# Kernel optimization log

Hardware: AMD Instinct MI355X
Metric: run time of the kernel (lower is better)

The kernel has to match this reference:

```python
import jax, jax.numpy as jnp
import numpy as np

N_NODES = 50000
N_EDGES = 800000
N_GRAPHS = 128
D = 128
L = 4
C = 10
GN_EPS = 1e-5


def setup_inputs() -> dict:
    key = jax.random.key(0)
    ks = jax.random.split(key, 12)
    s = 0.05
    x = jax.random.normal(ks[0], (N_NODES, D), dtype=jnp.float32)
    gin_w1 = jax.random.normal(ks[1], (L, D, D), dtype=jnp.float32) * s
    gin_b1 = jax.random.normal(ks[2], (L, D), dtype=jnp.float32) * s
    gin_w2 = jax.random.normal(ks[3], (L, D, D), dtype=jnp.float32) * s
    gin_b2 = jax.random.normal(ks[4], (L, D), dtype=jnp.float32) * s
    gn_weight = jnp.ones((L, D), dtype=jnp.float32)
    gn_bias = jnp.zeros((L, D), dtype=jnp.float32)
    gn_scale = jnp.ones((L, D), dtype=jnp.float32)
    fw1 = jax.random.normal(ks[5], (D, D), dtype=jnp.float32) * s
    fb1 = jnp.zeros((D,), dtype=jnp.float32)
    fw2 = jax.random.normal(ks[6], (D, D), dtype=jnp.float32) * s
    fb2 = jnp.zeros((D,), dtype=jnp.float32)
    fw3 = jax.random.normal(ks[7], (D, C), dtype=jnp.float32) * s
    fb3 = jnp.zeros((C,), dtype=jnp.float32)
    edge_index = jax.random.randint(ks[8], (2, N_EDGES), 0, N_NODES, dtype=jnp.int64)
    batch = jnp.sort(jax.random.randint(ks[9], (N_NODES,), 0, N_GRAPHS, dtype=jnp.int64))
    return dict(x=x, gin_w1=gin_w1, gin_b1=gin_b1, gin_w2=gin_w2, gin_b2=gin_b2,
                gn_weight=gn_weight, gn_bias=gn_bias, gn_scale=gn_scale,
                fw1=fw1, fb1=fb1, fw2=fw2, fb2=fb2, fw3=fw3, fb3=fb3,
                edge_index=edge_index, batch=batch)


def _graph_norm(h, batch, weight, bias, mean_scale, counts):
    # PyG GraphNorm: per-graph mean/var with learnable mean_scale.
    mean = jax.ops.segment_sum(h, batch, num_segments=N_GRAPHS) / counts  # [G, D]
    out = h - mean[batch] * mean_scale
    var = jax.ops.segment_sum(out * out, batch, num_segments=N_GRAPHS) / counts
    return weight * out / jnp.sqrt(var[batch] + GN_EPS) + bias


def reference(x, gin_w1, gin_b1, gin_w2, gin_b2, gn_weight, gn_bias, gn_scale,
              fw1, fb1, fw2, fb2, fw3, fb3, edge_index, batch):
    src, dst = edge_index[0], edge_index[1]
    ones = jnp.ones((N_NODES, 1), dtype=x.dtype)
    counts = jnp.maximum(jax.ops.segment_sum(ones, batch, num_segments=N_GRAPHS), 1.0)  # [G,1]
    h = x
    for l in range(L):
        # GINConv, eps=0: (1+eps)*x + sum_{j->i} x_j, then MLP with act after each Linear
        agg = jax.ops.segment_sum(h[src], dst, num_segments=N_NODES)  # [N, D]
        h = h + agg
        h = jax.nn.relu(h @ gin_w1[l] + gin_b1[l])
        h = jax.nn.relu(h @ gin_w2[l] + gin_b2[l])
        h = _graph_norm(h, batch, gn_weight[l], gn_bias[l], gn_scale[l], counts)
        h = jax.nn.relu(h)
    # sum readout per graph
    g = jax.ops.segment_sum(h, batch, num_segments=N_GRAPHS)  # [G, D]
    # final MLP (dropout is identity in eval)
    g = jax.nn.relu(g @ fw1 + fb1)
    g = jax.nn.relu(g @ fw2 + fb2)
    out = g @ fw3 + fb3
    return jax.nn.log_softmax(out, axis=-1)
```

## Files before the change

kernel.cpp:

```cpp
#include <hip/hip_runtime.h>
#include <cstddef>

#define N_NODES 50000
#define N_EDGES 800000
#define N_GRAPHS 128
#define DIM 128
#define N_LAYERS 4
#define GN_EPS 1e-5f

#define B_CHUNK 256
#define EPB 3125
#define BUCKET_SHIFT 9
#define BUCKET_SIZE 512
#define NB 98

#define CX_BLKS 12500
#define CW_BLKS 512
#define GB_BLKS 196
#define SETUP_BLKS (CX_BLKS + CW_BLKS + GB_BLKS + B_CHUNK)

typedef unsigned short ushort_t;
typedef __attribute__((ext_vector_type(8))) short frag8;
typedef __attribute__((ext_vector_type(4))) float f32x4;

__device__ inline float bfbits2f(unsigned hi16) { return __uint_as_float(hi16 << 16); }
__device__ inline ushort_t bf16rne(float v) {
    unsigned u = __float_as_uint(v);
    unsigned r = u + 0x7fff + ((u >> 16) & 1);
    return (ushort_t)(r >> 16);
}
__device__ inline unsigned packbf2(float a, float b) {
    return (unsigned)bf16rne(a) | ((unsigned)bf16rne(b) << 16);
}
__device__ inline void bf16split(float v, ushort_t& h, ushort_t& l) {
    ushort_t hi = bf16rne(v);
    float fh = __uint_as_float(((unsigned)hi) << 16);
    l = bf16rne(v - fh);
    h = hi;
}

__global__ __launch_bounds__(256) void setup_misc(const float* __restrict__ x, unsigned* __restrict__ Hb,
                                                  const float* __restrict__ w1, const float* __restrict__ w2,
                                                  ushort_t* __restrict__ whi, ushort_t* __restrict__ wlo,
                                                  const int* __restrict__ batch, int* __restrict__ gstart,
                                                  const int* __restrict__ edst, int* __restrict__ cnts) {
    __shared__ int cnt[NB];
    int b = blockIdx.x, t = threadIdx.x;
    if (b < CX_BLKS) {
        int i = b * 256 + t;
        if (i < N_NODES * 64) {
            float a = x[2 * i], bb = x[2 * i + 1];
            Hb[i] = packbf2(a, bb);
        }
    } else if (b < CX_BLKS + CW_BLKS) {
        int idx = (b - CX_BLKS) * 256 + t;
        int mat = idx >> 14;
        int e = idx & 16383;
        int n = e >> 7, k = e & 127;
        int l = mat >> 1;
        const float* src = (mat & 1) ? (w2 + (size_t)l * DIM * DIM) : (w1 + (size_t)l * DIM * DIM);
        float v = src[k * DIM + n];
        ushort_t h, lw;
        bf16split(v, h, lw);
        whi[(size_t)mat * DIM * DIM + n * DIM + k] = h;
        wlo[(size_t)mat * DIM * DIM + n * DIM + k] = lw;
    } else if (b < CX_BLKS + CW_BLKS + GB_BLKS) {
        int i = (b - CX_BLKS - CW_BLKS) * 256 + t;
        if (i < N_NODES) {
            int bb = batch[i];
            if (i == 0) {
                for (int g = 0; g <= bb; ++g) gstart[g] = 0;
            } else {
                int pb = batch[i - 1];
                for (int g = pb + 1; g <= bb; ++g) gstart[g] = i;
            }
            if (i == N_NODES - 1) {
                for (int g = bb + 1; g <= N_GRAPHS; ++g) gstart[g] = N_NODES;
            }
        }
    } else {
        int blk = b - (CX_BLKS + CW_BLKS + GB_BLKS);
        for (int i = t; i < NB; i += 256) cnt[i] = 0;
        __syncthreads();
        int base = blk * EPB;
        for (int i = t; i < EPB; i += 256) atomicAdd(&cnt[edst[base + i] >> BUCKET_SHIFT], 1);
        __syncthreads();
        for (int i = t; i < NB; i += 256) cnts[i * B_CHUNK + blk] = cnt[i];
    }
}

__global__ __launch_bounds__(1024) void scan_local(const int* __restrict__ in, int* __restrict__ out,
                                                   int* __restrict__ bsum, int n) {
    __shared__ int wsum[16];
    int tid = threadIdx.x, lane = tid & 63, w = tid >> 6;
    int gi = blockIdx.x * 1024 + tid;
    int v = (gi < n) ? in[gi] : 0;
    int s = v;
    #pragma unroll
    for (int off = 1; off < 64; off <<= 1) {
        int t = __shfl_up(s, off, 64);
        if (lane >= off) s += t;
    }
    if (lane == 63) wsum[w] = s;
    __syncthreads();
    if (w == 0) {
        int ws = (lane < 16) ? wsum[lane] : 0;
        #pragma unroll
        for (int off = 1; off < 16; off <<= 1) {
            int t = __shfl_up(ws, off, 64);
            if (lane >= off) ws += t;
        }
        if (lane < 16) wsum[lane] = ws;
    }
    __syncthreads();
    int woff = (w > 0) ? wsum[w - 1] : 0;
    if (gi < n) out[gi] = woff + s - v;
    if (tid == 1023) bsum[blockIdx.x] = woff + s;
}

__global__ __launch_bounds__(1024) void scan_add(int* __restrict__ out, const int* __restrict__ bsum,
                                                 int n, int total) {
    int lane = threadIdx.x & 63;
    int v = (lane < (int)blockIdx.x) ? bsum[lane] : 0;
    #pragma unroll
    for (int off = 1; off < 64; off <<= 1) v += __shfl_xor(v, off, 64);
    int gi = blockIdx.x * 1024 + threadIdx.x;
    if (gi < n) out[gi] += v;
    if (blockIdx.x == 0 && threadIdx.x == 0) out[n] = total;
}

__global__ __launch_bounds__(256) void p3_place(const int* __restrict__ src, const int* __restrict__ dst,
                                                const int* __restrict__ off, unsigned* __restrict__ ebuf) {
    __shared__ int cur[NB];
    int t = threadIdx.x, blk = blockIdx.x;
    for (int i = t; i < NB; i += 256) cur[i] = off[i * B_CHUNK + blk];
    __syncthreads();
    int base = blk * EPB;
    for (int i = t; i < EPB; i += 256) {
        int d = dst[base + i];
        int b = d >> BUCKET_SHIFT;
        int pos = atomicAdd(&cur[b], 1);
        ebuf[pos] = (unsigned)src[base + i] | ((unsigned)(d & (BUCKET_SIZE - 1)) << 16);
    }
}

__global__ __launch_bounds__(512) void p4_csr(const unsigned* __restrict__ ebuf, const int* __restrict__ off,
                                              int* __restrict__ eoff, int* __restrict__ csr) {
    __shared__ int cnt[BUCKET_SIZE];
    __shared__ int wsum[8];
    int k = blockIdx.x, t = threadIdx.x;
    int bstart = off[k * B_CHUNK];
    int bend = off[(k + 1) * B_CHUNK];
    cnt[t] = 0;
    __syncthreads();
    for (int i = bstart + t; i < bend; i += 512) atomicAdd(&cnt[ebuf[i] >> 16], 1);
    __syncthreads();
    int lane = t & 63, w = t >> 6;
    int v = cnt[t], s = v;
    #pragma unroll
    for (int o = 1; o < 64; o <<= 1) {
        int tt = __shfl_up(s, o, 64);
        if (lane >= o) s += tt;
    }
    if (lane == 63) wsum[w] = s;
    __syncthreads();
    if (w == 0) {
        int ws = (lane < 8) ? wsum[lane] : 0;
        #pragma unroll
        for (int o = 1; o < 8; o <<= 1) {
            int tt = __shfl_up(ws, o, 64);
            if (lane >= o) ws += tt;
        }
        if (lane < 8) wsum[lane] = ws;
    }
    __syncthreads();
    int woff = (w > 0) ? wsum[w - 1] : 0;
    int excl = woff + s - v;
    int node = k * BUCKET_SIZE + t;
    if (node < N_NODES) eoff[node] = bstart + excl;
    __syncthreads();
    cnt[t] = excl;
    __syncthreads();
    for (int i = bstart + t; i < bend; i += 512) {
        unsigned p = ebuf[i];
        int pos = atomicAdd(&cnt[p >> 16], 1);
        csr[bstart + pos] = (int)(p & 0xffffu);
    }
    if (k == NB - 1 && t == 0) eoff[N_NODES] = N_EDGES;
}

__global__ __launch_bounds__(256) void agg_bf16(const uint4* __restrict__ h4, const int* __restrict__ eoff,
                                                const int* __restrict__ csr, uint4* __restrict__ T4) {
    int wid = (blockIdx.x * 256 + threadIdx.x) >> 6;
    int lane = threadIdx.x & 63;
    int qtr = lane >> 4;
    int ql = lane & 15;
    if (wid >= N_NODES) return;
    int lo = eoff[wid], hi = eoff[wid + 1];

    float a[8];
    #pragma unroll
    for (int k = 0; k < 8; ++k) a[k] = 0.f;

    auto acc_row = [&](uint4 w) {
        a[0] += bfbits2f(w.x & 0xffffu); a[1] += bfbits2f(w.x >> 16);
        a[2] += bfbits2f(w.y & 0xffffu); a[3] += bfbits2f(w.y >> 16);
        a[4] += bfbits2f(w.z & 0xffffu); a[5] += bfbits2f(w.z >> 16);
        a[6] += bfbits2f(w.w & 0xffffu); a[7] += bfbits2f(w.w >> 16);
    };

    if (qtr == 0) acc_row(h4[(size_t)wid * 16 + ql]);

    for (int base = lo; base < hi; base += 64) {
        int nav = hi - base;
        if (nav > 64) nav = 64;
        int jv = (base + lane < hi) ? csr[base + lane] : 0;
        int cmin = nav >> 2;
        int cmax = (nav + 3) >> 2;
        int i = 0;
        for (; i + 3 < cmin; i += 4) {
            int j0 = __shfl(jv, 4 * (i + 0) + qtr, 64);
            int j1 = __shfl(jv, 4 * (i + 1) + qtr, 64);
            int j2 = __shfl(jv, 4 * (i + 2) + qtr, 64);
            int j3 = __shfl(jv, 4 * (i + 3) + qtr, 64);
            uint4 w0 = h4[(size_t)j0 * 16 + ql];
            uint4 w1 = h4[(size_t)j1 * 16 + ql];
            uint4 w2 = h4[(size_t)j2 * 16 + ql];
            uint4 w3 = h4[(size_t)j3 * 16 + ql];
            acc_row(w0); acc_row(w1); acc_row(w2); acc_row(w3);
        }
        for (; i < cmin; ++i) {
            int j = __shfl(jv, 4 * i + qtr, 64);
            acc_row(h4[(size_t)j * 16 + ql]);
        }
        for (; i < cmax; ++i) {
            int epos = 4 * i + qtr;
            int j = __shfl(jv, epos, 64);
            if (epos < nav) acc_row(h4[(size_t)j * 16 + ql]);
        }
    }

    #pragma unroll
    for (int k = 0; k < 8; ++k) {
        a[k] += __shfl_down(a[k], 32, 64);
        a[k] += __shfl_down(a[k], 16, 64);
    }
    if (qtr == 0) {
        uint4 o;
        o.x = packbf2(a[0], a[1]);
        o.y = packbf2(a[2], a[3]);
        o.z = packbf2(a[4], a[5]);
        o.w = packbf2(a[6], a[7]);
        T4[(size_t)wid * 16 + ql] = o;
    }
}

__global__ __launch_bounds__(512) void mm_layer(const ushort_t* __restrict__ A,
                                                const ushort_t* __restrict__ W1h, const ushort_t* __restrict__ W1l,
                                                const ushort_t* __restrict__ W2h, const ushort_t* __restrict__ W2l,
                                                const float* __restrict__ b1, const float* __restrict__ b2,
                                                ushort_t* __restrict__ Zb) {
    __shared__ ushort_t As[256 * 128];
    __shared__ ushort_t Ws[128 * 128];
    int tid = threadIdx.x;
    int row0 = blockIdx.x * 256;
    int wave = tid >> 6, lane = tid & 63;
    int q = lane >> 4, mn = lane & 15;

    f32x4 acc[2][8];
    #pragma unroll
    for (int t = 0; t < 2; ++t)
        #pragma unroll
        for (int n = 0; n < 8; ++n) acc[t][n] = (f32x4)(0.f);

    #pragma unroll
    for (int i = 0; i < 8; ++i) {
        int c = tid + i * 512;
        int r = c >> 4, c8 = c & 15;
        uint4 v = make_uint4(0u, 0u, 0u, 0u);
        int gr = row0 + r;
        if (gr < N_NODES) v = *(const uint4*)(A + (size_t)gr * DIM + c8 * 8);
        *(uint4*)(&As[r * 128 + (c8 ^ (r & 7)) * 8]) = v;
    }
    auto stageW = [&](const ushort_t* src) {
        #pragma unroll
        for (int i = 0; i < 4; ++i) {
            int c = tid + i * 512;
            int r = c >> 4, c8 = c & 15;
            uint4 v = *(const uint4*)(src + r * DIM + c8 * 8);
            *(uint4*)(&Ws[r * 128 + (c8 ^ (r & 7)) * 8]) = v;
        }
    };
    auto compute = [&]() {
        #pragma unroll
        for (int ks = 0; ks < 4; ++ks) {
            int m0 = wave * 32 + mn;
            int m1 = m0 + 16;
            frag8 a0 = *(const frag8*)&As[m0 * 128 + (((ks * 4 + q) ^ (m0 & 7)) * 8)];
            frag8 a1 = *(const frag8*)&As[m1 * 128 + (((ks * 4 + q) ^ (m1 & 7)) * 8)];
            #pragma unroll
            for (int n = 0; n < 8; ++n) {
                int nr = n * 16 + mn;
                frag8 b = *(const frag8*)&Ws[nr * 128 + (((ks * 4 + q) ^ (nr & 7)) * 8)];
                acc[0][n] = __builtin_amdgcn_mfma_f32_16x16x32_bf16(a0, b, acc[0][n], 0, 0, 0);
                acc[1][n] = __builtin_amdgcn_mfma_f32_16x16x32_bf16(a1, b, acc[1][n], 0, 0, 0);
            }
        }
    };

    stageW(W1h);
    __syncthreads(); compute(); __syncthreads();
    stageW(W1l);
    __syncthreads(); compute(); __syncthreads();

    int mloc = wave * 32;
    #pragma unroll
    for (int t = 0; t < 2; ++t) {
        #pragma unroll
        for (int n = 0; n < 8; ++n) {
            int col = n * 16 + mn;
            float bv = b1[col];
            #pragma unroll
            for (int r = 0; r < 4; ++r) {
                int rloc = mloc + t * 16 + q * 4 + r;
                float v = fmaxf(acc[t][n][r] + bv, 0.f);
                As[rloc * 128 + ((col >> 3) ^ (rloc & 7)) * 8 + (col & 7)] = bf16rne(v);
                acc[t][n][r] = 0.f;
            }
        }
    }
    __syncthreads();
    stageW(W2h);
    __syncthreads(); compute(); __syncthreads();
    stageW(W2l);
    __syncthreads(); compute();

    #pragma unroll
    for (int t = 0; t < 2; ++t) {
        #pragma unroll
        for (int n = 0; n < 8; ++n) {
            int col = n * 16 + mn;
            float bv = b2[col];
            #pragma unroll
            for (int r = 0; r < 4; ++r) {
                int grow = row0 + mloc + t * 16 + q * 4 + r;
                if (grow < N_NODES)
                    Zb[(size_t)grow * DIM + col] = bf16rne(fmaxf(acc[t][n][r] + bv, 0.f));
            }
        }
    }
}

__global__ __launch_bounds__(1024) void gn_fused(const unsigned* __restrict__ Zb, const int* __restrict__ gstart,
                                                 const float* __restrict__ scale, const float* __restrict__ weight,
                                                 const float* __restrict__ bias,
                                                 unsigned* __restrict__ Hb) {
    __shared__ float2 sh1[1024], sh2[1024];
    __shared__ float sa[64], sb[64];
    int g = blockIdx.x >> 1, half = blockIdx.x & 1;
    int dpl = threadIdx.x & 31, rg = threadIdx.x >> 5;
    int dp = half * 32 + dpl;
    int s = gstart[g], e = gstart[g + 1];
    float2 s1 = make_float2(0.f, 0.f), s2 = make_float2(0.f, 0.f);
    for (int n = s + rg; n < e; n += 32) {
        unsigned zz = Zb[(size_t)n * 64 + dp];
        float z0 = bfbits2f(zz & 0xffffu), z1 = bfbits2f(zz >> 16);
        s1.x += z0; s1.y += z1;
        s2.x += z0 * z0; s2.y += z1 * z1;
    }
    sh1[threadIdx.x] = s1;
    sh2[threadIdx.x] = s2;
    __syncthreads();
    if (rg == 0) {
        #pragma unroll
        for (int k = 1; k < 32; ++k) {
            float2 t1 = sh1[dpl + 32 * k], t2 = sh2[dpl + 32 * k];
            s1.x += t1.x; s1.y += t1.y;
            s2.x += t2.x; s2.y += t2.y;
        }
        int cnt = e - s;
        float cf = (float)(cnt > 0 ? cnt : 1);
        int d0 = dp * 2, d1 = d0 + 1;
        float m0 = s1.x / cf, m1 = s1.y / cf;
        float ez0 = s2.x / cf, ez1 = s2.y / cf;
        float sc0 = scale[d0], sc1 = scale[d1];
        float var0 = fmaxf(ez0 - (2.0f - sc0) * sc0 * m0 * m0, 0.f);
        float var1 = fmaxf(ez1 - (2.0f - sc1) * sc1 * m1 * m1, 0.f);
        sa[dpl * 2] = m0 * sc0;
        sa[dpl * 2 + 1] = m1 * sc1;
        sb[dpl * 2] = weight[d0] / sqrtf(var0 + GN_EPS);
        sb[dpl * 2 + 1] = weight[d1] / sqrtf(var1 + GN_EPS);
    }
    __syncthreads();
    float as0 = sa[dpl * 2], bm0 = sb[dpl * 2], bi0 = bias[dp * 2];
    float as1 = sa[dpl * 2 + 1], bm1 = sb[dpl * 2 + 1], bi1 = bias[dp * 2 + 1];
    for (int n = s + rg; n < e; n += 32) {
        unsigned zz = Zb[(size_t)n * 64 + dp];
        float z0 = bfbits2f(zz & 0xffffu), z1 = bfbits2f(zz >> 16);
        float o0 = fmaxf((z0 - as0) * bm0 + bi0, 0.f);
        float o1 = fmaxf((z1 - as1) * bm1 + bi1, 0.f);
        Hb[(size_t)n * 64 + dp] = packbf2(o0, o1);
    }
}

__global__ __launch_bounds__(1024) void gn_last(const unsigned* __restrict__ Zb, const int* __restrict__ gstart,
                                                const float* __restrict__ scale, const float* __restrict__ weight,
                                                const float* __restrict__ bias,
                                                const float* __restrict__ fw1, const float* __restrict__ fb1,
                                                const float* __restrict__ fw2, const float* __restrict__ fb2,
                                                const float* __restrict__ fw3, const float* __restrict__ fb3,
                                                float* __restrict__ out) {
    __shared__ float2 sh1[1024], sh2[1024];
    __shared__ float sa[128], sb[128];
    __shared__ float v0[128], v1[128], v2[128], lg[10];
    int g = blockIdx.x;
    int t = threadIdx.x;
    int dp = t & 63, rg = t >> 6;
    int s = gstart[g], e = gstart[g + 1];
    float2 s1 = make_float2(0.f, 0.f), s2 = make_float2(0.f, 0.f);
    for (int n = s + rg; n < e; n += 16) {
        unsigned zz = Zb[(size_t)n * 64 + dp];
        float z0 = bfbits2f(zz & 0xffffu), z1 = bfbits2f(zz >> 16);
        s1.x += z0; s1.y += z1;
        s2.x += z0 * z0; s2.y += z1 * z1;
    }
    sh1[t] = s1;
    sh2[t] = s2;
    __syncthreads();
    if (rg == 0) {
        #pragma unroll
        for (int k = 1; k < 16; ++k) {
            float2 t1 = sh1[dp + 64 * k], t2 = sh2[dp + 64 * k];
            s1.x += t1.x; s1.y += t1.y;
            s2.x += t2.x; s2.y += t2.y;
        }
        int cnt = e - s;
        float cf = (float)(cnt > 0 ? cnt : 1);
        int d0 = dp * 2, d1 = d0 + 1;
        float m0 = s1.x / cf, m1 = s1.y / cf;
        float ez0 = s2.x / cf, ez1 = s2.y / cf;
        float sc0 = scale[d0], sc1 = scale[d1];
        float var0 = fmaxf(ez0 - (2.0f - sc0) * sc0 * m0 * m0, 0.f);
        float var1 = fmaxf(ez1 - (2.0f - sc1) * sc1 * m1 * m1, 0.f);
        sa[d0] = m0 * sc0;
        sa[d1] = m1 * sc1;
        sb[d0] = weight[d0] / sqrtf(var0 + GN_EPS);
        sb[d1] = weight[d1] / sqrtf(var1 + GN_EPS);
    }
    __syncthreads();
    int d0 = dp * 2, d1 = d0 + 1;
    float as0 = sa[d0], bm0 = sb[d0], bi0 = bias[d0];
    float as1 = sa[d1], bm1 = sb[d1], bi1 = bias[d1];
    float2 rsum = make_float2(0.f, 0.f);
    for (int n = s + rg; n < e; n += 16) {
        unsigned zz = Zb[(size_t)n * 64 + dp];
        float z0 = bfbits2f(zz & 0xffffu), z1 = bfbits2f(zz >> 16);
        rsum.x += fmaxf((z0 - as0) * bm0 + bi0, 0.f);
        rsum.y += fmaxf((z1 - as1) * bm1 + bi1, 0.f);
    }
    __syncthreads();
    sh1[t] = rsum;
    __syncthreads();
    if (rg == 0) {
        #pragma unroll
        for (int k = 1; k < 16; ++k) {
            float2 t1 = sh1[dp + 64 * k];
            rsum.x += t1.x; rsum.y += t1.y;
        }
        v0[d0] = rsum.x;
        v0[d1] = rsum.y;
    }
    __syncthreads();
    if (t < 128) {
        float acc = fb1[t];
        for (int d = 0; d < 128; ++d) acc += v0[d] * fw1[d * 128 + t];
        v1[t] = fmaxf(acc, 0.f);
    }
    __syncthreads();
    if (t < 128) {
        float acc = fb2[t];
        for (int d = 0; d < 128; ++d) acc += v1[d] * fw2[d * 128 + t];
        v2[t] = fmaxf(acc, 0.f);
    }
    __syncthreads();
    if (t < 10) {
        float acc = fb3[t];
        for (int d = 0; d < 128; ++d) acc += v2[d] * fw3[d * 10 + t];
        lg[t] = acc;
    }
    __syncthreads();
    if (t < 10) {
        float m = -1e30f;
        for (int c = 0; c < 10; ++c) m = fmaxf(m, lg[c]);
        float ssum = 0.f;
        for (int c = 0; c < 10; ++c) ssum += expf(lg[c] - m);
        out[g * 10 + t] = lg[t] - m - logf(ssum);
    }
}

extern "C" void kernel_launch(void* const* d_in, const int* in_sizes, int n_in,
                              void* d_out, int out_size, void* d_ws, size_t ws_size,
                              hipStream_t stream) {
    const float* x      = (const float*)d_in[0];
    const float* gin_w1 = (const float*)d_in[1];
    const float* gin_b1 = (const float*)d_in[2];
    const float* gin_w2 = (const float*)d_in[3];
    const float* gin_b2 = (const float*)d_in[4];
    const float* gn_w   = (const float*)d_in[5];
    const float* gn_b   = (const float*)d_in[6];
    const float* gn_s   = (const float*)d_in[7];
    const float* fw1    = (const float*)d_in[8];
    const float* fb1    = (const float*)d_in[9];
    const float* fw2    = (const float*)d_in[10];
    const float* fb2    = (const float*)d_in[11];
    const float* fw3    = (const float*)d_in[12];
    const float* fb3    = (const float*)d_in[13];
    const int*   eidx   = (const int*)d_in[14];
    const int*   batch  = (const int*)d_in[15];
    float* out = (float*)d_out;

    const int* esrc = eidx;
    const int* edst = eidx + N_EDGES;

    auto align_up = [](size_t v) { return (v + 255) & ~(size_t)255; };
    char* p = (char*)d_ws;
    unsigned* Hb = (unsigned*)p;   p += align_up((size_t)N_NODES * DIM * 2);
    unsigned* Tb = (unsigned*)p;   p += align_up((size_t)N_NODES * DIM * 2);
    unsigned* Zb = (unsigned*)p;   p += align_up((size_t)N_NODES * DIM * 2);
    ushort_t* WThi = (ushort_t*)p; p += align_up((size_t)8 * DIM * DIM * 2);
    ushort_t* WTlo = (ushort_t*)p; p += align_up((size_t)8 * DIM * DIM * 2);
    int* gstart = (int*)p;         p += align_up((N_GRAPHS + 1) * 4);
    int* cnts = (int*)p;           p += align_up((size_t)NB * B_CHUNK * 4);
    int* off = (int*)p;            p += align_up(((size_t)NB * B_CHUNK + 1) * 4);
    int* bsum = (int*)p;           p += align_up(64 * 4);
    unsigned* ebuf = (unsigned*)p; p += align_up((size_t)N_EDGES * 4);
    int* eoff = (int*)p;           p += align_up((N_NODES + 1) * 4);
    int* csr = (int*)p;            p += align_up((size_t)N_EDGES * 4);

    const int SCAN_N = NB * B_CHUNK;
    const int SCAN_BLKS = (SCAN_N + 1023) / 1024;
    setup_misc<<<SETUP_BLKS, 256, 0, stream>>>(x, Hb, gin_w1, gin_w2, WThi, WTlo,
                                               batch, gstart, edst, cnts);
    scan_local<<<SCAN_BLKS, 1024, 0, stream>>>(cnts, off, bsum, SCAN_N);
    scan_add<<<SCAN_BLKS, 1024, 0, stream>>>(off, bsum, SCAN_N, N_EDGES);
    p3_place<<<B_CHUNK, 256, 0, stream>>>(esrc, edst, off, ebuf);
    p4_csr<<<NB, 512, 0, stream>>>(ebuf, off, eoff, csr);

    const int mm_grid = (N_NODES + 255) / 256;
    for (int l = 0; l < N_LAYERS; ++l) {
        agg_bf16<<<(N_NODES + 3) / 4, 256, 0, stream>>>((const uint4*)Hb, eoff, csr, (uint4*)Tb);
        mm_layer<<<mm_grid, 512, 0, stream>>>((const ushort_t*)Tb,
            WThi + (size_t)(2 * l) * DIM * DIM, WTlo + (size_t)(2 * l) * DIM * DIM,
            WThi + (size_t)(2 * l + 1) * DIM * DIM, WTlo + (size_t)(2 * l + 1) * DIM * DIM,
            gin_b1 + l * DIM, gin_b2 + l * DIM, (ushort_t*)Zb);
        if (l == N_LAYERS - 1)
            gn_last<<<N_GRAPHS, 1024, 0, stream>>>(Zb, gstart, gn_s + l * DIM,
                gn_w + l * DIM, gn_b + l * DIM, fw1, fb1, fw2, fb2, fw3, fb3, out);
        else
            gn_fused<<<N_GRAPHS * 2, 1024, 0, stream>>>(Zb, gstart, gn_s + l * DIM,
                gn_w + l * DIM, gn_b + l * DIM, Hb);
    }
}
```

Measured before the change: 388.7 us.

## Fuse neighbor aggregation into the GIN MLP kernel and widen GraphNorm loads

```diff
diff --git a/kernel.cpp b/kernel.cpp
--- a/kernel.cpp
+++ b/kernel.cpp
@@ -18,6 +18,8 @@
 #define CW_BLKS 512
 #define GB_BLKS 196
 #define SETUP_BLKS (CX_BLKS + CW_BLKS + GB_BLKS + B_CHUNK)
+
+#define MM_BLKS 391
 
 typedef unsigned short ushort_t;
 typedef __attribute__((ext_vector_type(8))) short frag8;
@@ -189,99 +191,83 @@
     if (k == NB - 1 && t == 0) eoff[N_NODES] = N_EDGES;
 }
 
-__global__ __launch_bounds__(256) void agg_bf16(const uint4* __restrict__ h4, const int* __restrict__ eoff,
-                                                const int* __restrict__ csr, uint4* __restrict__ T4) {
-    int wid = (blockIdx.x * 256 + threadIdx.x) >> 6;
-    int lane = threadIdx.x & 63;
-    int qtr = lane >> 4;
-    int ql = lane & 15;
-    if (wid >= N_NODES) return;
-    int lo = eoff[wid], hi = eoff[wid + 1];
-
-    float a[8];
-    #pragma unroll
-    for (int k = 0; k < 8; ++k) a[k] = 0.f;
-
-    auto acc_row = [&](uint4 w) {
-        a[0] += bfbits2f(w.x & 0xffffu); a[1] += bfbits2f(w.x >> 16);
-        a[2] += bfbits2f(w.y & 0xffffu); a[3] += bfbits2f(w.y >> 16);
-        a[4] += bfbits2f(w.z & 0xffffu); a[5] += bfbits2f(w.z >> 16);
-        a[6] += bfbits2f(w.w & 0xffffu); a[7] += bfbits2f(w.w >> 16);
-    };
-
-    if (qtr == 0) acc_row(h4[(size_t)wid * 16 + ql]);
-
-    for (int base = lo; base < hi; base += 64) {
-        int nav = hi - base;
-        if (nav > 64) nav = 64;
-        int jv = (base + lane < hi) ? csr[base + lane] : 0;
-        int cmin = nav >> 2;
-        int cmax = (nav + 3) >> 2;
-        int i = 0;
-        for (; i + 3 < cmin; i += 4) {
-            int j0 = __shfl(jv, 4 * (i + 0) + qtr, 64);
-            int j1 = __shfl(jv, 4 * (i + 1) + qtr, 64);
-            int j2 = __shfl(jv, 4 * (i + 2) + qtr, 64);
-            int j3 = __shfl(jv, 4 * (i + 3) + qtr, 64);
-            uint4 w0 = h4[(size_t)j0 * 16 + ql];
-            uint4 w1 = h4[(size_t)j1 * 16 + ql];
-            uint4 w2 = h4[(size_t)j2 * 16 + ql];
-            uint4 w3 = h4[(size_t)j3 * 16 + ql];
-            acc_row(w0); acc_row(w1); acc_row(w2); acc_row(w3);
-        }
-        for (; i < cmin; ++i) {
-            int j = __shfl(jv, 4 * i + qtr, 64);
-            acc_row(h4[(size_t)j * 16 + ql]);
-        }
-        for (; i < cmax; ++i) {
-            int epos = 4 * i + qtr;
-            int j = __shfl(jv, epos, 64);
-            if (epos < nav) acc_row(h4[(size_t)j * 16 + ql]);
-        }
-    }
-
-    #pragma unroll
-    for (int k = 0; k < 8; ++k) {
-        a[k] += __shfl_down(a[k], 32, 64);
-        a[k] += __shfl_down(a[k], 16, 64);
-    }
-    if (qtr == 0) {
-        uint4 o;
-        o.x = packbf2(a[0], a[1]);
-        o.y = packbf2(a[2], a[3]);
-        o.z = packbf2(a[4], a[5]);
-        o.w = packbf2(a[6], a[7]);
-        T4[(size_t)wid * 16 + ql] = o;
-    }
-}
-
-__global__ __launch_bounds__(512) void mm_layer(const ushort_t* __restrict__ A,
-                                                const ushort_t* __restrict__ W1h, const ushort_t* __restrict__ W1l,
-                                                const ushort_t* __restrict__ W2h, const ushort_t* __restrict__ W2l,
-                                                const float* __restrict__ b1, const float* __restrict__ b2,
-                                                ushort_t* __restrict__ Zb) {
-    __shared__ ushort_t As[256 * 128];
+__global__ __launch_bounds__(512, 4) void mm_fused(const uint4* __restrict__ h4,
+                                                   const int* __restrict__ eoff, const int* __restrict__ csr,
+                                                   const ushort_t* __restrict__ W1h, const ushort_t* __restrict__ W1l,
+                                                   const ushort_t* __restrict__ W2h, const ushort_t* __restrict__ W2l,
+                                                   const float* __restrict__ b1, const float* __restrict__ b2,
+                                                   ushort_t* __restrict__ Zb) {
+    __shared__ ushort_t As[128 * 128];
     __shared__ ushort_t Ws[128 * 128];
     int tid = threadIdx.x;
-    int row0 = blockIdx.x * 256;
+    int row0 = blockIdx.x * 128;
     int wave = tid >> 6, lane = tid & 63;
-    int q = lane >> 4, mn = lane & 15;
-
-    f32x4 acc[2][8];
-    #pragma unroll
-    for (int t = 0; t < 2; ++t)
-        #pragma unroll
-        for (int n = 0; n < 8; ++n) acc[t][n] = (f32x4)(0.f);
-
-    #pragma unroll
-    for (int i = 0; i < 8; ++i) {
-        int c = tid + i * 512;
-        int r = c >> 4, c8 = c & 15;
-        uint4 v = make_uint4(0u, 0u, 0u, 0u);
-        int gr = row0 + r;
-        if (gr < N_NODES) v = *(const uint4*)(A + (size_t)gr * DIM + c8 * 8);
-        *(uint4*)(&As[r * 128 + (c8 ^ (r & 7)) * 8]) = v;
-    }
+    int qtr = lane >> 4, ql = lane & 15;
+
+    for (int i = 0; i < 16; ++i) {
+        int r = wave * 16 + i;
+        int node = row0 + r;
+        float a[8];
+        #pragma unroll
+        for (int k = 0; k < 8; ++k) a[k] = 0.f;
+        auto acc_row = [&](uint4 w) {
+            a[0] += bfbits2f(w.x & 0xffffu); a[1] += bfbits2f(w.x >> 16);
+            a[2] += bfbits2f(w.y & 0xffffu); a[3] += bfbits2f(w.y >> 16);
+            a[4] += bfbits2f(w.z & 0xffffu); a[5] += bfbits2f(w.z >> 16);
+            a[6] += bfbits2f(w.w & 0xffffu); a[7] += bfbits2f(w.w >> 16);
+        };
+        if (node < N_NODES) {
+            if (qtr == 0) acc_row(h4[(size_t)node * 16 + ql]);
+            int lo = eoff[node], hi = eoff[node + 1];
+            for (int base = lo; base < hi; base += 64) {
+                int nav = hi - base;
+                if (nav > 64) nav = 64;
+                int jv = (base + lane < hi) ? csr[base + lane] : 0;
+                int cmin = nav >> 2;
+                int cmax = (nav + 3) >> 2;
+                int ii = 0;
+                for (; ii + 3 < cmin; ii += 4) {
+                    int j0 = __shfl(jv, 4 * (ii + 0) + qtr, 64);
+                    int j1 = __shfl(jv, 4 * (ii + 1) + qtr, 64);
+                    int j2 = __shfl(jv, 4 * (ii + 2) + qtr, 64);
+                    int j3 = __shfl(jv, 4 * (ii + 3) + qtr, 64);
+                    uint4 w0 = h4[(size_t)j0 * 16 + ql];
+                    uint4 w1 = h4[(size_t)j1 * 16 + ql];
+                    uint4 w2 = h4[(size_t)j2 * 16 + ql];
+                    uint4 w3 = h4[(size_t)j3 * 16 + ql];
+                    acc_row(w0); acc_row(w1); acc_row(w2); acc_row(w3);
+                }
+                for (; ii < cmin; ++ii) {
+                    int j = __shfl(jv, 4 * ii + qtr, 64);
+                    acc_row(h4[(size_t)j * 16 + ql]);
+                }
+                for (; ii < cmax; ++ii) {
+                    int epos = 4 * ii + qtr;
+                    int j = __shfl(jv, epos, 64);
+                    if (epos < nav) acc_row(h4[(size_t)j * 16 + ql]);
+                }
+            }
+            #pragma unroll
+            for (int k = 0; k < 8; ++k) {
+                a[k] += __shfl_down(a[k], 32, 64);
+                a[k] += __shfl_down(a[k], 16, 64);
+            }
+        }
+        if (qtr == 0) {
+            uint4 o;
+            o.x = packbf2(a[0], a[1]);
+            o.y = packbf2(a[2], a[3]);
+            o.z = packbf2(a[4], a[5]);
+            o.w = packbf2(a[6], a[7]);
+            *(uint4*)(&As[r * 128 + ((ql ^ (r & 7)) * 8)]) = o;
+        }
+    }
+
+    int q = qtr, mn = ql;
+    f32x4 acc[8];
+    #pragma unroll
+    for (int n = 0; n < 8; ++n) acc[n] = (f32x4)(0.f);
+
     auto stageW = [&](const ushort_t* src) {
         #pragma unroll
         for (int i = 0; i < 4; ++i) {
@@ -294,16 +280,13 @@
     auto compute = [&]() {
         #pragma unroll
         for (int ks = 0; ks < 4; ++ks) {
-            int m0 = wave * 32 + mn;
-            int m1 = m0 + 16;
+            int m0 = wave * 16 + mn;
             frag8 a0 = *(const frag8*)&As[m0 * 128 + (((ks * 4 + q) ^ (m0 & 7)) * 8)];
-            frag8 a1 = *(const frag8*)&As[m1 * 128 + (((ks * 4 + q) ^ (m1 & 7)) * 8)];
             #pragma unroll
             for (int n = 0; n < 8; ++n) {
                 int nr = n * 16 + mn;
                 frag8 b = *(const frag8*)&Ws[nr * 128 + (((ks * 4 + q) ^ (nr & 7)) * 8)];
-                acc[0][n] = __builtin_amdgcn_mfma_f32_16x16x32_bf16(a0, b, acc[0][n], 0, 0, 0);
-                acc[1][n] = __builtin_amdgcn_mfma_f32_16x16x32_bf16(a1, b, acc[1][n], 0, 0, 0);
+                acc[n] = __builtin_amdgcn_mfma_f32_16x16x32_bf16(a0, b, acc[n], 0, 0, 0);
             }
         }
     };
@@ -313,20 +296,17 @@
     stageW(W1l);
     __syncthreads(); compute(); __syncthreads();
 
-    int mloc = wave * 32;
-    #pragma unroll
-    for (int t = 0; t < 2; ++t) {
-        #pragma unroll
-        for (int n = 0; n < 8; ++n) {
-            int col = n * 16 + mn;
-            float bv = b1[col];
-            #pragma unroll
-            for (int r = 0; r < 4; ++r) {
-                int rloc = mloc + t * 16 + q * 4 + r;
-                float v = fmaxf(acc[t][n][r] + bv, 0.f);
-                As[rloc * 128 + ((col >> 3) ^ (rloc & 7)) * 8 + (col & 7)] = bf16rne(v);
-                acc[t][n][r] = 0.f;
-            }
+    int mloc = wave * 16;
+    #pragma unroll
+    for (int n = 0; n < 8; ++n) {
+        int col = n * 16 + mn;
+        float bv = b1[col];
+        #pragma unroll
+        for (int r = 0; r < 4; ++r) {
+            int rloc = mloc + q * 4 + r;
+            float v = fmaxf(acc[n][r] + bv, 0.f);
+            As[rloc * 128 + ((col >> 3) ^ (rloc & 7)) * 8 + (col & 7)] = bf16rne(v);
+            acc[n][r] = 0.f;
         }
     }
     __syncthreads();
@@ -336,17 +316,14 @@
     __syncthreads(); compute();
 
     #pragma unroll
-    for (int t = 0; t < 2; ++t) {
-        #pragma unroll
-        for (int n = 0; n < 8; ++n) {
-            int col = n * 16 + mn;
-            float bv = b2[col];
-            #pragma unroll
-            for (int r = 0; r < 4; ++r) {
-                int grow = row0 + mloc + t * 16 + q * 4 + r;
-                if (grow < N_NODES)
-                    Zb[(size_t)grow * DIM + col] = bf16rne(fmaxf(acc[t][n][r] + bv, 0.f));
-            }
+    for (int n = 0; n < 8; ++n) {
+        int col = n * 16 + mn;
+        float bv = b2[col];
+        #pragma unroll
+        for (int r = 0; r < 4; ++r) {
+            int grow = row0 + mloc + q * 4 + r;
+            if (grow < N_NODES)
+                Zb[(size_t)grow * DIM + col] = bf16rne(fmaxf(acc[n][r] + bv, 0.f));
         }
     }
 }
@@ -355,51 +332,57 @@
                                                  const float* __restrict__ scale, const float* __restrict__ weight,
                                                  const float* __restrict__ bias,
                                                  unsigned* __restrict__ Hb) {
-    __shared__ float2 sh1[1024], sh2[1024];
+    __shared__ f32x4 sh1[1024], sh2[1024];
     __shared__ float sa[64], sb[64];
     int g = blockIdx.x >> 1, half = blockIdx.x & 1;
-    int dpl = threadIdx.x & 31, rg = threadIdx.x >> 5;
-    int dp = half * 32 + dpl;
+    int t = threadIdx.x;
+    int uld = t & 15, rg = t >> 4;
     int s = gstart[g], e = gstart[g + 1];
-    float2 s1 = make_float2(0.f, 0.f), s2 = make_float2(0.f, 0.f);
-    for (int n = s + rg; n < e; n += 32) {
-        unsigned zz = Zb[(size_t)n * 64 + dp];
-        float z0 = bfbits2f(zz & 0xffffu), z1 = bfbits2f(zz >> 16);
-        s1.x += z0; s1.y += z1;
-        s2.x += z0 * z0; s2.y += z1 * z1;
-    }
-    sh1[threadIdx.x] = s1;
-    sh2[threadIdx.x] = s2;
-    __syncthreads();
+    const unsigned* zp = Zb + half * 32 + uld * 2;
+    f32x4 s1 = (f32x4)(0.f), s2 = (f32x4)(0.f);
+    for (int n = s + rg; n < e; n += 64) {
+        uint2 zz = *(const uint2*)(zp + (size_t)n * 64);
+        f32x4 z;
+        z[0] = bfbits2f(zz.x & 0xffffu); z[1] = bfbits2f(zz.x >> 16);
+        z[2] = bfbits2f(zz.y & 0xffffu); z[3] = bfbits2f(zz.y >> 16);
+        s1 += z;
+        s2 += z * z;
+    }
+    sh1[t] = s1;
+    sh2[t] = s2;
+    __syncthreads();
+    int dbase = half * 64 + uld * 4;
     if (rg == 0) {
-        #pragma unroll
-        for (int k = 1; k < 32; ++k) {
-            float2 t1 = sh1[dpl + 32 * k], t2 = sh2[dpl + 32 * k];
-            s1.x += t1.x; s1.y += t1.y;
-            s2.x += t2.x; s2.y += t2.y;
-        }
+        #pragma unroll 8
+        for (int k = 1; k < 64; ++k) { s1 += sh1[uld + 16 * k]; s2 += sh2[uld + 16 * k]; }
         int cnt = e - s;
         float cf = (float)(cnt > 0 ? cnt : 1);
-        int d0 = dp * 2, d1 = d0 + 1;
-        float m0 = s1.x / cf, m1 = s1.y / cf;
-        float ez0 = s2.x / cf, ez1 = s2.y / cf;
-        float sc0 = scale[d0], sc1 = scale[d1];
-        float var0 = fmaxf(ez0 - (2.0f - sc0) * sc0 * m0 * m0, 0.f);
-        float var1 = fmaxf(ez1 - (2.0f - sc1) * sc1 * m1 * m1, 0.f);
-        sa[dpl * 2] = m0 * sc0;
-        sa[dpl * 2 + 1] = m1 * sc1;
-        sb[dpl * 2] = weight[d0] / sqrtf(var0 + GN_EPS);
-        sb[dpl * 2 + 1] = weight[d1] / sqrtf(var1 + GN_EPS);
-    }
-    __syncthreads();
-    float as0 = sa[dpl * 2], bm0 = sb[dpl * 2], bi0 = bias[dp * 2];
-    float as1 = sa[dpl * 2 + 1], bm1 = sb[dpl * 2 + 1], bi1 = bias[dp * 2 + 1];
-    for (int n = s + rg; n < e; n += 32) {
-        unsigned zz = Zb[(size_t)n * 64 + dp];
-        float z0 = bfbits2f(zz & 0xffffu), z1 = bfbits2f(zz >> 16);
+        #pragma unroll
+        for (int j = 0; j < 4; ++j) {
+            float m = s1[j] / cf, ez = s2[j] / cf;
+            float sc = scale[dbase + j];
+            float var = fmaxf(ez - (2.0f - sc) * sc * m * m, 0.f);
+            sa[uld * 4 + j] = m * sc;
+            sb[uld * 4 + j] = weight[dbase + j] / sqrtf(var + GN_EPS);
+        }
+    }
+    __syncthreads();
+    float as0 = sa[uld * 4], as1 = sa[uld * 4 + 1], as2 = sa[uld * 4 + 2], as3 = sa[uld * 4 + 3];
+    float bm0 = sb[uld * 4], bm1 = sb[uld * 4 + 1], bm2 = sb[uld * 4 + 2], bm3 = sb[uld * 4 + 3];
+    float bi0 = bias[dbase], bi1 = bias[dbase + 1], bi2 = bias[dbase + 2], bi3 = bias[dbase + 3];
+    unsigned* hp = Hb + half * 32 + uld * 2;
+    for (int n = s + rg; n < e; n += 64) {
+        uint2 zz = *(const uint2*)(zp + (size_t)n * 64);
+        float z0 = bfbits2f(zz.x & 0xffffu), z1 = bfbits2f(zz.x >> 16);
+        float z2 = bfbits2f(zz.y & 0xffffu), z3 = bfbits2f(zz.y >> 16);
         float o0 = fmaxf((z0 - as0) * bm0 + bi0, 0.f);
         float o1 = fmaxf((z1 - as1) * bm1 + bi1, 0.f);
-        Hb[(size_t)n * 64 + dp] = packbf2(o0, o1);
+        float o2 = fmaxf((z2 - as2) * bm2 + bi2, 0.f);
+        float o3 = fmaxf((z3 - as3) * bm3 + bi3, 0.f);
+        uint2 o;
+        o.x = packbf2(o0, o1);
+        o.y = packbf2(o2, o3);
+        *(uint2*)(hp + (size_t)n * 64) = o;
     }
 }
 
@@ -410,65 +393,67 @@
                                                 const float* __restrict__ fw2, const float* __restrict__ fb2,
                                                 const float* __restrict__ fw3, const float* __restrict__ fb3,
                                                 float* __restrict__ out) {
-    __shared__ float2 sh1[1024], sh2[1024];
+    __shared__ f32x4 sh1[1024], sh2[1024];
     __shared__ float sa[128], sb[128];
     __shared__ float v0[128], v1[128], v2[128], lg[10];
     int g = blockIdx.x;
     int t = threadIdx.x;
-    int dp = t & 63, rg = t >> 6;
+    int du = t & 31, rg = t >> 5;
     int s = gstart[g], e = gstart[g + 1];
-    float2 s1 = make_float2(0.f, 0.f), s2 = make_float2(0.f, 0.f);
-    for (int n = s + rg; n < e; n += 16) {
-        unsigned zz = Zb[(size_t)n * 64 + dp];
-        float z0 = bfbits2f(zz & 0xffffu), z1 = bfbits2f(zz >> 16);
-        s1.x += z0; s1.y += z1;
-        s2.x += z0 * z0; s2.y += z1 * z1;
+    const unsigned* zp = Zb + du * 2;
+    f32x4 s1 = (f32x4)(0.f), s2 = (f32x4)(0.f);
+    for (int n = s + rg; n < e; n += 32) {
+        uint2 zz = *(const uint2*)(zp + (size_t)n * 64);
+        f32x4 z;
+        z[0] = bfbits2f(zz.x & 0xffffu); z[1] = bfbits2f(zz.x >> 16);
+        z[2] = bfbits2f(zz.y & 0xffffu); z[3] = bfbits2f(zz.y >> 16);
+        s1 += z;
+        s2 += z * z;
     }
     sh1[t] = s1;
     sh2[t] = s2;
     __syncthreads();
+    int dbase = du * 4;
     if (rg == 0) {
-        #pragma unroll
-        for (int k = 1; k < 16; ++k) {
-            float2 t1 = sh1[dp + 64 * k], t2 = sh2[dp + 64 * k];
-            s1.x += t1.x; s1.y += t1.y;
-            s2.x += t2.x; s2.y += t2.y;
-        }
+        #pragma unroll 8
+        for (int k = 1; k < 32; ++k) { s1 += sh1[du + 32 * k]; s2 += sh2[du + 32 * k]; }
         int cnt = e - s;
         float cf = (float)(cnt > 0 ? cnt : 1);
-        int d0 = dp * 2, d1 = d0 + 1;
-        float m0 = s1.x / cf, m1 = s1.y / cf;
-        float ez0 = s2.x / cf, ez1 = s2.y / cf;
-        float sc0 = scale[d0], sc1 = scale[d1];
-        float var0 = fmaxf(ez0 - (2.0f - sc0) * sc0 * m0 * m0, 0.f);
-        float var1 = fmaxf(ez1 - (2.0f - sc1) * sc1 * m1 * m1, 0.f);
-        sa[d0] = m0 * sc0;
-        sa[d1] = m1 * sc1;
-        sb[d0] = weight[d0] / sqrtf(var0 + GN_EPS);
-        sb[d1] = weight[d1] / sqrtf(var1 + GN_EPS);
-    }
-    __syncthreads();
-    int d0 = dp * 2, d1 = d0 + 1;
-    float as0 = sa[d0], bm0 = sb[d0], bi0 = bias[d0];
-    float as1 = sa[d1], bm1 = sb[d1], bi1 = bias[d1];
-    float2 rsum = make_float2(0.f, 0.f);
-    for (int n = s + rg; n < e; n += 16) {
-        unsigned zz = Zb[(size_t)n * 64 + dp];
-        float z0 = bfbits2f(zz & 0xffffu), z1 = bfbits2f(zz >> 16);
-        rsum.x += fmaxf((z0 - as0) * bm0 + bi0, 0.f);
-        rsum.y += fmaxf((z1 - as1) * bm1 + bi1, 0.f);
+        #pragma unroll
+        for (int j = 0; j < 4; ++j) {
+            float m = s1[j] / cf, ez = s2[j] / cf;
+            float sc = scale[dbase + j];
+            float var = fmaxf(ez - (2.0f - sc) * sc * m * m, 0.f);
+            sa[dbase + j] = m * sc;
+            sb[dbase + j] = weight[dbase + j] / sqrtf(var + GN_EPS);
+        }
+    }
+    __syncthreads();
+    float as_[4], bm_[4], bi_[4];
+    #pragma unroll
+    for (int j = 0; j < 4; ++j) {
+        as_[j] = sa[dbase + j];
+        bm_[j] = sb[dbase + j];
+        bi_[j] = bias[dbase + j];
+    }
+    f32x4 rsum = (f32x4)(0.f);
+    for (int n = s + rg; n < e; n += 32) {
+        uint2 zz = *(const uint2*)(zp + (size_t)n * 64);
+        float z0 = bfbits2f(zz.x & 0xffffu), z1 = bfbits2f(zz.x >> 16);
+        float z2 = bfbits2f(zz.y & 0xffffu), z3 = bfbits2f(zz.y >> 16);
+        rsum[0] += fmaxf((z0 - as_[0]) * bm_[0] + bi_[0], 0.f);
+        rsum[1] += fmaxf((z1 - as_[1]) * bm_[1] + bi_[1], 0.f);
+        rsum[2] += fmaxf((z2 - as_[2]) * bm_[2] + bi_[2], 0.f);
+        rsum[3] += fmaxf((z3 - as_[3]) * bm_[3] + bi_[3], 0.f);
     }
     __syncthreads();
     sh1[t] = rsum;
     __syncthreads();
     if (rg == 0) {
-        #pragma unroll
-        for (int k = 1; k < 16; ++k) {
-            float2 t1 = sh1[dp + 64 * k];
-            rsum.x += t1.x; rsum.y += t1.y;
-        }
-        v0[d0] = rsum.x;
-        v0[d1] = rsum.y;
+        #pragma unroll 8
+        for (int k = 1; k < 32; ++k) rsum += sh1[du + 32 * k];
+        #pragma unroll
+        for (int j = 0; j < 4; ++j) v0[dbase + j] = rsum[j];
     }
     __syncthreads();
     if (t < 128) {
@@ -525,7 +510,6 @@
     auto align_up = [](size_t v) { return (v + 255) & ~(size_t)255; };
     char* p = (char*)d_ws;
     unsigned* Hb = (unsigned*)p;   p += align_up((size_t)N_NODES * DIM * 2);
-    unsigned* Tb = (unsigned*)p;   p += align_up((size_t)N_NODES * DIM * 2);
     unsigned* Zb = (unsigned*)p;   p += align_up((size_t)N_NODES * DIM * 2);
     ushort_t* WThi = (ushort_t*)p; p += align_up((size_t)8 * DIM * DIM * 2);
     ushort_t* WTlo = (ushort_t*)p; p += align_up((size_t)8 * DIM * DIM * 2);
@@ -546,10 +530,8 @@
     p3_place<<<B_CHUNK, 256, 0, stream>>>(esrc, edst, off, ebuf);
     p4_csr<<<NB, 512, 0, stream>>>(ebuf, off, eoff, csr);
 
-    const int mm_grid = (N_NODES + 255) / 256;
     for (int l = 0; l < N_LAYERS; ++l) {
-        agg_bf16<<<(N_NODES + 3) / 4, 256, 0, stream>>>((const uint4*)Hb, eoff, csr, (uint4*)Tb);
-        mm_layer<<<mm_grid, 512, 0, stream>>>((const ushort_t*)Tb,
+        mm_fused<<<MM_BLKS, 512, 0, stream>>>((const uint4*)Hb, eoff, csr,
             WThi + (size_t)(2 * l) * DIM * DIM, WTlo + (size_t)(2 * l) * DIM * DIM,
             WThi + (size_t)(2 * l + 1) * DIM * DIM, WTlo + (size_t)(2 * l + 1) * DIM * DIM,
             gin_b1 + l * DIM, gin_b2 + l * DIM, (ushort_t*)Zb);
```

Result: slower. 451.4 us (+16.1%).
